# Kernel optimization log

Hardware: AMD Instinct MI355X
Metric: run time of the kernel (lower is better)

Reference implementation:

```python
import jax, jax.numpy as jnp
import numpy as np

B, S, D, H, N = 8, 1024, 1024, 16, 16  # batch, seq, hidden, heads, num_ns_tokens
HD = D // H


def setup_inputs() -> dict:
    key = jax.random.key(0)
    ks = jax.random.split(key, 8)
    s = 0.02
    return {
        "x": jax.random.normal(ks[0], (B, S, D), jnp.float32),
        "Wq_shared": jax.random.normal(ks[1], (D, D), jnp.float32) * s,
        "Wk_shared": jax.random.normal(ks[2], (D, D), jnp.float32) * s,
        "Wv_shared": jax.random.normal(ks[3], (D, D), jnp.float32) * s,
        "Wq_ded": jax.random.normal(ks[4], (N, D, D), jnp.float32) * s,
        "Wk_ded": jax.random.normal(ks[5], (N, D, D), jnp.float32) * s,
        "Wv_ded": jax.random.normal(ks[6], (N, D, D), jnp.float32) * s,
        "Wo": jax.random.normal(ks[7], (D, D), jnp.float32) * s,
    }


def reference(x, Wq_shared, Wk_shared, Wv_shared, Wq_ded, Wk_ded, Wv_ded, Wo):
    b, s, d = x.shape
    n = Wq_ded.shape[0]

    def proj(Ws, Wd):
        shared = x @ Ws                                   # [b,s,d]
        ded = jnp.einsum('bnd,ndo->bno', x[:, :n], Wd)    # first n tokens use dedicated weights
        return jnp.concatenate([ded, shared[:, n:]], axis=1)

    q = proj(Wq_shared, Wq_ded).reshape(b, s, H, HD)
    k = proj(Wk_shared, Wk_ded).reshape(b, s, H, HD)
    v = proj(Wv_shared, Wv_ded).reshape(b, s, H, HD)

    scores = jnp.einsum('bqhd,bkhd->bhqk', q, k) / jnp.sqrt(jnp.float32(HD))
    causal = jnp.tril(jnp.ones((s, s), dtype=bool))
    scores = jnp.where(causal, scores, jnp.float32(-1e9))
    attn = jax.nn.softmax(scores, axis=-1)
    out = jnp.einsum('bhqk,bkhd->bqhd', attn, v).reshape(b, s, d)
    output = out @ Wo
    return (output, k, v)
```

## Files before the change

### kernel.cpp

```cpp
#include <hip/hip_runtime.h>
#include <cstdint>


typedef unsigned short u16;
typedef __attribute__((ext_vector_type(8)))  __bf16 bf16x8;
typedef __attribute__((ext_vector_type(8)))  u16    u16x8;
typedef __attribute__((ext_vector_type(4)))  float  f32x4;

#define LOG2E 1.4426950408889634f
#define BSD   (8u * 1024u * 1024u)

__device__ __forceinline__ u16 f2bf(float f) {
    unsigned u = __builtin_bit_cast(unsigned, f);
    u += 0x7fffu + ((u >> 16) & 1u);
    return (u16)(u >> 16);
}

__device__ __forceinline__ void gl_lds16(const void* g, void* l) {
    __builtin_amdgcn_global_load_lds(
        (const __attribute__((address_space(1))) unsigned*)g,
        (__attribute__((address_space(3))) unsigned*)l, 16, 0, 0);
}

__global__ __launch_bounds__(256) void wt_convert(
        const float* __restrict__ Wq, const float* __restrict__ Wk,
        const float* __restrict__ Wv, const float* __restrict__ Wo,
        u16* __restrict__ WTcat, u16* __restrict__ WoT) {
    int z = blockIdx.z;
    const float* src = (z == 0) ? Wq : (z == 1) ? Wk : (z == 2) ? Wv : Wo;
    u16* dst = (z < 3) ? (WTcat + (size_t)z * 1024 * 1024) : WoT;
    int k0 = blockIdx.x * 32, n0 = blockIdx.y * 32;
    __shared__ float t[32][33];
    int x = threadIdx.x & 31, y = threadIdx.x >> 5;
#pragma unroll
    for (int i = 0; i < 4; ++i)
        t[y + 8 * i][x] = src[(size_t)(k0 + y + 8 * i) * 1024 + n0 + x];
    __syncthreads();
#pragma unroll
    for (int i = 0; i < 4; ++i)
        dst[(size_t)(n0 + y + 8 * i) * 1024 + k0 + x] = f2bf(t[x][y + 8 * i]);
}

__global__ __launch_bounds__(256) void x_convert(
        const float4* __restrict__ x, u16* __restrict__ xb) {
    int i = blockIdx.x * 256 + threadIdx.x;
    float4 v = x[i];
    ushort4 o;
    o.x = f2bf(v.x); o.y = f2bf(v.y); o.z = f2bf(v.z); o.w = f2bf(v.w);
    ((ushort4*)xb)[i] = o;
}

template <int MODE>
__global__ __launch_bounds__(256) void gemm128(
        const u16* __restrict__ A, const u16* __restrict__ Bt,
        float* __restrict__ fout, u16* __restrict__ q_attn,
        u16* __restrict__ k_attn, u16* __restrict__ vT) {
    const int K = 1024;
    __shared__ u16 As[128 * 32];
    __shared__ u16 Bs[128 * 32];
    int tid = threadIdx.x;
    int wave = tid >> 6, lane = tid & 63;
    int m0 = blockIdx.y * 128, n0 = blockIdx.x * 128;
    int wm = wave & 1, wn = wave >> 1;
    int lr = lane & 15, kg = lane >> 4;

    f32x4 acc[4][4] = {};

    int ci0 = wave * 128 + lane;
    int ci1 = ci0 + 64;

    for (int k0 = 0; k0 < K; k0 += 32) {
        __syncthreads();
        {
            int ci = ci0, row = ci >> 2, cg = (ci & 3) ^ ((row >> 1) & 3);
            gl_lds16(A  + (size_t)(m0 + row) * K + k0 + cg * 8, As + ci * 8);
            gl_lds16(Bt + (size_t)(n0 + row) * K + k0 + cg * 8, Bs + ci * 8);
            ci = ci1; row = ci >> 2; cg = (ci & 3) ^ ((row >> 1) & 3);
            gl_lds16(A  + (size_t)(m0 + row) * K + k0 + cg * 8, As + ci * 8);
            gl_lds16(Bt + (size_t)(n0 + row) * K + k0 + cg * 8, Bs + ci * 8);
        }
        __syncthreads();
        bf16x8 af[4], bf[4];
#pragma unroll
        for (int i = 0; i < 4; ++i) {
            int row = wm * 64 + i * 16 + lr;
            af[i] = __builtin_bit_cast(bf16x8,
                *(const u16x8*)&As[row * 32 + ((kg ^ ((row >> 1) & 3)) * 8)]);
        }
#pragma unroll
        for (int j = 0; j < 4; ++j) {
            int row = wn * 64 + j * 16 + lr;
            bf[j] = __builtin_bit_cast(bf16x8,
                *(const u16x8*)&Bs[row * 32 + ((kg ^ ((row >> 1) & 3)) * 8)]);
        }
#pragma unroll
        for (int i = 0; i < 4; ++i)
#pragma unroll
            for (int j = 0; j < 4; ++j)
                acc[i][j] = __builtin_amdgcn_mfma_f32_16x16x32_bf16(
                    af[i], bf[j], acc[i][j], 0, 0, 0);
    }

    if (MODE == 1) {
#pragma unroll
        for (int i = 0; i < 4; ++i) {
            int mbase = m0 + wm * 64 + i * 16 + kg * 4;
#pragma unroll
            for (int j = 0; j < 4; ++j) {
                int col = n0 + wn * 64 + j * 16 + lr;
#pragma unroll
                for (int r = 0; r < 4; ++r)
                    fout[(size_t)(mbase + r) * 1024 + col] = acc[i][j][r];
            }
        }
    } else {
        int matId = n0 >> 10;
        int ncol0 = (n0 & 1023) + wn * 64;
#pragma unroll
        for (int i = 0; i < 4; ++i) {
            int mbase = m0 + wm * 64 + i * 16 + kg * 4;
#pragma unroll
            for (int j = 0; j < 4; ++j) {
                int col = ncol0 + j * 16 + lr;
                int h = col >> 6, hd = col & 63;
#pragma unroll
                for (int r = 0; r < 4; ++r) {
                    int mm = mbase + r;
                    int b = mm >> 10, s = mm & 1023;
                    float v = acc[i][j][r];
                    size_t aidx = ((size_t)((b * 16 + h) * 1024 + s)) * 64 + hd;
                    if (matId == 0) {
                        q_attn[aidx] = f2bf(v * 0.125f);
                    } else if (matId == 1) {
                        fout[(size_t)BSD + (size_t)mm * 1024 + col] = v;
                        k_attn[aidx] = f2bf(v);
                    } else {
                        fout[(size_t)2 * BSD + (size_t)mm * 1024 + col] = v;
                        vT[((size_t)((b * 16 + h) * 64 + hd)) * 1024 + s] = f2bf(v);
                    }
                }
            }
        }
    }
}

__global__ __launch_bounds__(256) void ded_partial(
        const float* __restrict__ x, const float* __restrict__ Wq,
        const float* __restrict__ Wk, const float* __restrict__ Wv,
        float* __restrict__ part) {
    int dc = blockIdx.x, n = blockIdx.y, mat = blockIdx.z;
    const float* W = ((mat == 0) ? Wq : (mat == 1) ? Wk : Wv) +
                     (size_t)n * 1024 * 1024;
    __shared__ float xs[8 * 128];
    int t = threadIdx.x;
    for (int i = t; i < 1024; i += 256) {
        int b = i >> 7, d = i & 127;
        xs[i] = x[((size_t)b * 1024 + n) * 1024 + dc * 128 + d];
    }
    __syncthreads();
    int o0 = t * 4;
    float4 acc[8];
#pragma unroll
    for (int b = 0; b < 8; ++b) acc[b] = make_float4(0.f, 0.f, 0.f, 0.f);
    for (int d = 0; d < 128; ++d) {
        float4 w = *(const float4*)&W[(size_t)(dc * 128 + d) * 1024 + o0];
#pragma unroll
        for (int b = 0; b < 8; ++b) {
            float xv = xs[b * 128 + d];
            acc[b].x += xv * w.x; acc[b].y += xv * w.y;
            acc[b].z += xv * w.z; acc[b].w += xv * w.w;
        }
    }
#pragma unroll
    for (int b = 0; b < 8; ++b)
        *(float4*)&part[(size_t)(((mat * 8 + dc) * 8 + b) * 16 + n) * 1024 + o0] = acc[b];
}

__global__ __launch_bounds__(256) void ded_fixup(
        const float* __restrict__ part, float* __restrict__ d_out,
        u16* __restrict__ q_attn, u16* __restrict__ k_attn,
        u16* __restrict__ vT) {
    int blk = blockIdx.x;
    int mat = blk >> 7, b = (blk >> 4) & 7, n = blk & 15;
    int o0 = threadIdx.x * 4;
    float v[4] = {0.f, 0.f, 0.f, 0.f};
    for (int dc = 0; dc < 8; ++dc) {
        float4 p = *(const float4*)&part[(size_t)(((mat * 8 + dc) * 8 + b) * 16 + n) * 1024 + o0];
        v[0] += p.x; v[1] += p.y; v[2] += p.z; v[3] += p.w;
    }
#pragma unroll
    for (int j = 0; j < 4; ++j) {
        int col = o0 + j, h = col >> 6, hd = col & 63;
        size_t aidx = ((size_t)((b * 16 + h) * 1024 + n)) * 64 + hd;
        if (mat == 0) {
            q_attn[aidx] = f2bf(v[j] * 0.125f);
        } else if (mat == 1) {
            d_out[(size_t)BSD + ((size_t)b * 1024 + n) * 1024 + col] = v[j];
            k_attn[aidx] = f2bf(v[j]);
        } else {
            d_out[(size_t)2 * BSD + ((size_t)b * 1024 + n) * 1024 + col] = v[j];
            vT[((size_t)((b * 16 + h) * 64 + hd)) * 1024 + n] = f2bf(v[j]);
        }
    }
}

__global__ __launch_bounds__(256) void attn(
        const u16* __restrict__ q_attn, const u16* __restrict__ k_attn,
        const u16* __restrict__ vT, u16* __restrict__ O) {
    int qt = blockIdx.x, h = blockIdx.y, b = blockIdx.z;
    const u16* Qg = q_attn + (((size_t)(b * 16 + h) * 1024) + qt * 128) * 64;
    const u16* Kg = k_attn + ((size_t)(b * 16 + h) * 1024) * 64;
    const u16* Vg = vT + (size_t)(b * 16 + h) * 64 * 1024;

    __shared__ u16 Qs[128 * 64];
    __shared__ u16 Ks[64 * 64];
    __shared__ u16 Vs[64 * 64];
    __shared__ u16 Ps[128 * 64];
    __shared__ float red[4 * 32];

    int tid = threadIdx.x, wave = tid >> 6, lane = tid & 63;
    int lr = lane & 15, kg = lane >> 4;

#pragma unroll
    for (int j = 0; j < 4; ++j) {
        int ci = j * 256 + tid;
        int row = ci >> 3, cg = (ci & 7) ^ (row & 7);
        gl_lds16(Qg + (size_t)row * 64 + cg * 8, Qs + ci * 8);
    }

    float m_run[2] = {-1e30f, -1e30f};
    float l_run[2] = {0.f, 0.f};
    f32x4 oacc[2][4] = {};

    int nkt = 2 * qt + 2;
    for (int kt = 0; kt < nkt; ++kt) {
        __syncthreads();
#pragma unroll
        for (int j = 0; j < 2; ++j) {
            int ci = j * 256 + tid;
            int row = ci >> 3, cg = (ci & 7) ^ (row & 7);
            gl_lds16(Kg + ((size_t)(kt * 64 + row)) * 64 + cg * 8, Ks + ci * 8);
            gl_lds16(Vg + (size_t)row * 1024 + kt * 64 + cg * 8, Vs + ci * 8);
        }
        __syncthreads();

        f32x4 sacc[4][2] = {};
#pragma unroll
        for (int ks = 0; ks < 2; ++ks) {
            bf16x8 af[4], bq[2];
#pragma unroll
            for (int mi = 0; mi < 4; ++mi) {
                int row = mi * 16 + lr;
                af[mi] = __builtin_bit_cast(bf16x8,
                    *(const u16x8*)&Ks[row * 64 + (((ks * 4 + kg) ^ (row & 7)) * 8)]);
            }
#pragma unroll
            for (int nj = 0; nj < 2; ++nj) {
                int qr = wave * 32 + nj * 16 + lr;
                bq[nj] = __builtin_bit_cast(bf16x8,
                    *(const u16x8*)&Qs[qr * 64 + (((ks * 4 + kg) ^ (qr & 7)) * 8)]);
            }
#pragma unroll
            for (int mi = 0; mi < 4; ++mi)
#pragma unroll
                for (int nj = 0; nj < 2; ++nj)
                    sacc[mi][nj] = __builtin_amdgcn_mfma_f32_16x16x32_bf16(
                        af[mi], bq[nj], sacc[mi][nj], 0, 0, 0);
        }

        if (kt >= 2 * qt) {
#pragma unroll
            for (int mi = 0; mi < 4; ++mi)
#pragma unroll
                for (int nj = 0; nj < 2; ++nj)
#pragma unroll
                    for (int r = 0; r < 4; ++r) {
                        int kk_g = kt * 64 + mi * 16 + kg * 4 + r;
                        int q_g  = qt * 128 + wave * 32 + nj * 16 + lr;
                        if (kk_g > q_g) sacc[mi][nj][r] = -1e30f;
                    }
        }

        float alpha[2];
#pragma unroll
        for (int nj = 0; nj < 2; ++nj) {
            float mx = -1e30f;
#pragma unroll
            for (int mi = 0; mi < 4; ++mi)
#pragma unroll
                for (int r = 0; r < 4; ++r) mx = fmaxf(mx, sacc[mi][nj][r]);
            mx = fmaxf(mx, __shfl_xor(mx, 16));
            mx = fmaxf(mx, __shfl_xor(mx, 32));
            float mn = fmaxf(m_run[nj], mx);
            alpha[nj] = __builtin_amdgcn_exp2f((m_run[nj] - mn) * LOG2E);
            m_run[nj] = mn;
            float ps = 0.f;
            int q = wave * 32 + nj * 16 + lr;
#pragma unroll
            for (int mi = 0; mi < 4; ++mi) {
                float p0 = __builtin_amdgcn_exp2f((sacc[mi][nj][0] - mn) * LOG2E);
                float p1 = __builtin_amdgcn_exp2f((sacc[mi][nj][1] - mn) * LOG2E);
                float p2 = __builtin_amdgcn_exp2f((sacc[mi][nj][2] - mn) * LOG2E);
                float p3 = __builtin_amdgcn_exp2f((sacc[mi][nj][3] - mn) * LOG2E);
                ps += p0 + p1 + p2 + p3;
                int kkc = mi * 2 + (kg >> 1);
                int off = q * 64 + ((kkc ^ (q & 7)) * 8) + (kg & 1) * 4;
                uint2 w2;
                w2.x = (unsigned)f2bf(p0) | ((unsigned)f2bf(p1) << 16);
                w2.y = (unsigned)f2bf(p2) | ((unsigned)f2bf(p3) << 16);
                *(uint2*)&Ps[off] = w2;
            }
            ps += __shfl_xor(ps, 16);
            ps += __shfl_xor(ps, 32);
            l_run[nj] = l_run[nj] * alpha[nj] + ps;
            if (kg == 0) red[wave * 32 + nj * 16 + lr] = alpha[nj];
        }

#pragma unroll
        for (int mi = 0; mi < 2; ++mi) {
            f32x4 av = *(f32x4*)&red[wave * 32 + mi * 16 + kg * 4];
#pragma unroll
            for (int nj = 0; nj < 4; ++nj)
#pragma unroll
                for (int r = 0; r < 4; ++r) oacc[mi][nj][r] *= av[r];
        }
#pragma unroll
        for (int ks = 0; ks < 2; ++ks) {
            bf16x8 ap[2], bv[4];
#pragma unroll
            for (int mi = 0; mi < 2; ++mi) {
                int q = wave * 32 + mi * 16 + lr;
                ap[mi] = __builtin_bit_cast(bf16x8,
                    *(const u16x8*)&Ps[q * 64 + (((ks * 4 + kg) ^ (q & 7)) * 8)]);
            }
#pragma unroll
            for (int nj = 0; nj < 4; ++nj) {
                int hd = nj * 16 + lr;
                bv[nj] = __builtin_bit_cast(bf16x8,
                    *(const u16x8*)&Vs[hd * 64 + (((ks * 4 + kg) ^ (hd & 7)) * 8)]);
            }
#pragma unroll
            for (int mi = 0; mi < 2; ++mi)
#pragma unroll
                for (int nj = 0; nj < 4; ++nj)
                    oacc[mi][nj] = __builtin_amdgcn_mfma_f32_16x16x32_bf16(
                        ap[mi], bv[nj], oacc[mi][nj], 0, 0, 0);
        }
    }

    if (kg == 0) {
        red[wave * 32 + lr] = l_run[0];
        red[wave * 32 + 16 + lr] = l_run[1];
    }
#pragma unroll
    for (int mi = 0; mi < 2; ++mi) {
        f32x4 lv = *(f32x4*)&red[wave * 32 + mi * 16 + kg * 4];
        f32x4 rv;
#pragma unroll
        for (int r = 0; r < 4; ++r) rv[r] = __builtin_amdgcn_rcpf(lv[r]);
#pragma unroll
        for (int nj = 0; nj < 4; ++nj)
#pragma unroll
            for (int r = 0; r < 4; ++r) {
                int q_local = wave * 32 + mi * 16 + kg * 4 + r;
                size_t row = (size_t)b * 1024 + qt * 128 + q_local;
                O[row * 1024 + h * 64 + nj * 16 + lr] =
                    f2bf(oacc[mi][nj][r] * rv[r]);
            }
    }
}

extern "C" void kernel_launch(void* const* d_in, const int* in_sizes, int n_in,
                              void* d_out, int out_size, void* d_ws, size_t ws_size,
                              hipStream_t stream) {
    const float* x   = (const float*)d_in[0];
    const float* Wq  = (const float*)d_in[1];
    const float* Wk  = (const float*)d_in[2];
    const float* Wv  = (const float*)d_in[3];
    const float* Wqd = (const float*)d_in[4];
    const float* Wkd = (const float*)d_in[5];
    const float* Wvd = (const float*)d_in[6];
    const float* Wo  = (const float*)d_in[7];
    float* out = (float*)d_out;

    char* ws = (char*)d_ws;
    u16*   WTcat  = (u16*)(ws);
    u16*   WoT    = (u16*)(ws + 6291456);
    u16*   xb     = (u16*)(ws + 8388608);
    u16*   q_attn = (u16*)(ws + 25165824);
    u16*   k_attn = (u16*)(ws + 41943040);
    u16*   vT     = (u16*)(ws + 58720256);
    u16*   Ow     = (u16*)(ws + 75497472);
    float* part   = (float*)(ws + 92274688);

    wt_convert<<<dim3(32, 32, 4), 256, 0, stream>>>(Wq, Wk, Wv, Wo, WTcat, WoT);
    x_convert<<<dim3(8192), 256, 0, stream>>>((const float4*)x, xb);
    gemm128<0><<<dim3(24, 64), 256, 0, stream>>>(xb, WTcat, out, q_attn, k_attn, vT);
    ded_partial<<<dim3(8, 16, 3), 256, 0, stream>>>(x, Wqd, Wkd, Wvd, part);
    ded_fixup<<<dim3(384), 256, 0, stream>>>(part, out, q_attn, k_attn, vT);
    attn<<<dim3(8, 16, 8), 256, 0, stream>>>(q_attn, k_attn, vT, Ow);
    gemm128<1><<<dim3(8, 64), 256, 0, stream>>>(Ow, WoT, out, nullptr, nullptr, nullptr);
}
```

Before: 542.4 us.

## Move V transpose to separate kernel, fold log2e into Q scale, skip masked waves

```diff
diff --git a/kernel.cpp b/kernel.cpp
--- a/kernel.cpp
+++ b/kernel.cpp
@@ -7,8 +7,8 @@
 typedef __attribute__((ext_vector_type(8)))  u16    u16x8;
 typedef __attribute__((ext_vector_type(4)))  float  f32x4;
 
-#define LOG2E 1.4426950408889634f
 #define BSD   (8u * 1024u * 1024u)
+#define QSCALE 0.18033688011112042f
 
 __device__ __forceinline__ u16 f2bf(float f) {
     unsigned u = __builtin_bit_cast(unsigned, f);
@@ -54,7 +54,7 @@
 __global__ __launch_bounds__(256) void gemm128(
         const u16* __restrict__ A, const u16* __restrict__ Bt,
         float* __restrict__ fout, u16* __restrict__ q_attn,
-        u16* __restrict__ k_attn, u16* __restrict__ vT) {
+        u16* __restrict__ k_attn) {
     const int K = 1024;
     __shared__ u16 As[128 * 32];
     __shared__ u16 Bs[128 * 32];
@@ -130,13 +130,12 @@
                     float v = acc[i][j][r];
                     size_t aidx = ((size_t)((b * 16 + h) * 1024 + s)) * 64 + hd;
                     if (matId == 0) {
-                        q_attn[aidx] = f2bf(v * 0.125f);
+                        q_attn[aidx] = f2bf(v * QSCALE);
                     } else if (matId == 1) {
                         fout[(size_t)BSD + (size_t)mm * 1024 + col] = v;
                         k_attn[aidx] = f2bf(v);
                     } else {
                         fout[(size_t)2 * BSD + (size_t)mm * 1024 + col] = v;
-                        vT[((size_t)((b * 16 + h) * 64 + hd)) * 1024 + s] = f2bf(v);
                     }
                 }
             }
@@ -178,8 +177,7 @@
 
 __global__ __launch_bounds__(256) void ded_fixup(
         const float* __restrict__ part, float* __restrict__ d_out,
-        u16* __restrict__ q_attn, u16* __restrict__ k_attn,
-        u16* __restrict__ vT) {
+        u16* __restrict__ q_attn, u16* __restrict__ k_attn) {
     int blk = blockIdx.x;
     int mat = blk >> 7, b = (blk >> 4) & 7, n = blk & 15;
     int o0 = threadIdx.x * 4;
@@ -193,21 +191,51 @@
         int col = o0 + j, h = col >> 6, hd = col & 63;
         size_t aidx = ((size_t)((b * 16 + h) * 1024 + n)) * 64 + hd;
         if (mat == 0) {
-            q_attn[aidx] = f2bf(v[j] * 0.125f);
+            q_attn[aidx] = f2bf(v[j] * QSCALE);
         } else if (mat == 1) {
             d_out[(size_t)BSD + ((size_t)b * 1024 + n) * 1024 + col] = v[j];
             k_attn[aidx] = f2bf(v[j]);
         } else {
             d_out[(size_t)2 * BSD + ((size_t)b * 1024 + n) * 1024 + col] = v[j];
-            vT[((size_t)((b * 16 + h) * 64 + hd)) * 1024 + n] = f2bf(v[j]);
-        }
+        }
+    }
+}
+
+__global__ __launch_bounds__(256) void v_transpose(
+        const float* __restrict__ vf, u16* __restrict__ vT) {
+    int st = blockIdx.x, h = blockIdx.y, b = blockIdx.z;
+    __shared__ float t[64][65];
+    int tid = threadIdx.x;
+    int cg = tid & 15, sl = tid >> 4;
+#pragma unroll
+    for (int p = 0; p < 4; ++p) {
+        int s = p * 16 + sl;
+        float4 v = *(const float4*)&vf[
+            ((size_t)(b * 1024 + st * 64 + s)) * 1024 + h * 64 + cg * 4];
+        t[cg * 4 + 0][s] = v.x;
+        t[cg * 4 + 1][s] = v.y;
+        t[cg * 4 + 2][s] = v.z;
+        t[cg * 4 + 3][s] = v.w;
+    }
+    __syncthreads();
+    int hd = tid >> 2, sc = (tid & 3) * 16;
+    u16* dst = vT + ((size_t)((b * 16 + h) * 64 + hd)) * 1024 + st * 64 + sc;
+#pragma unroll
+    for (int c = 0; c < 4; ++c) {
+        ushort4 o;
+        o.x = f2bf(t[hd][sc + c * 4 + 0]);
+        o.y = f2bf(t[hd][sc + c * 4 + 1]);
+        o.z = f2bf(t[hd][sc + c * 4 + 2]);
+        o.w = f2bf(t[hd][sc + c * 4 + 3]);
+        *(ushort4*)(dst + c * 4) = o;
     }
 }
 
 __global__ __launch_bounds__(256) void attn(
         const u16* __restrict__ q_attn, const u16* __restrict__ k_attn,
         const u16* __restrict__ vT, u16* __restrict__ O) {
-    int qt = blockIdx.x, h = blockIdx.y, b = blockIdx.z;
+    int qt = 7 - blockIdx.x;
+    int h = blockIdx.y, b = blockIdx.z;
     const u16* Qg = q_attn + (((size_t)(b * 16 + h) * 1024) + qt * 128) * 64;
     const u16* Kg = k_attn + ((size_t)(b * 16 + h) * 1024) * 64;
     const u16* Vg = vT + (size_t)(b * 16 + h) * 64 * 1024;
@@ -244,107 +272,110 @@
         }
         __syncthreads();
 
-        f32x4 sacc[4][2] = {};
-#pragma unroll
-        for (int ks = 0; ks < 2; ++ks) {
-            bf16x8 af[4], bq[2];
-#pragma unroll
-            for (int mi = 0; mi < 4; ++mi) {
-                int row = mi * 16 + lr;
-                af[mi] = __builtin_bit_cast(bf16x8,
-                    *(const u16x8*)&Ks[row * 64 + (((ks * 4 + kg) ^ (row & 7)) * 8)]);
-            }
+        bool wactive = (qt * 128 + wave * 32 + 31) >= kt * 64;
+        if (wactive) {
+            f32x4 sacc[4][2] = {};
+#pragma unroll
+            for (int ks = 0; ks < 2; ++ks) {
+                bf16x8 af[4], bq[2];
+#pragma unroll
+                for (int mi = 0; mi < 4; ++mi) {
+                    int row = mi * 16 + lr;
+                    af[mi] = __builtin_bit_cast(bf16x8,
+                        *(const u16x8*)&Ks[row * 64 + (((ks * 4 + kg) ^ (row & 7)) * 8)]);
+                }
+#pragma unroll
+                for (int nj = 0; nj < 2; ++nj) {
+                    int qr = wave * 32 + nj * 16 + lr;
+                    bq[nj] = __builtin_bit_cast(bf16x8,
+                        *(const u16x8*)&Qs[qr * 64 + (((ks * 4 + kg) ^ (qr & 7)) * 8)]);
+                }
+#pragma unroll
+                for (int mi = 0; mi < 4; ++mi)
+#pragma unroll
+                    for (int nj = 0; nj < 2; ++nj)
+                        sacc[mi][nj] = __builtin_amdgcn_mfma_f32_16x16x32_bf16(
+                            af[mi], bq[nj], sacc[mi][nj], 0, 0, 0);
+            }
+
+            if (kt >= 2 * qt) {
+#pragma unroll
+                for (int mi = 0; mi < 4; ++mi)
+#pragma unroll
+                    for (int nj = 0; nj < 2; ++nj)
+#pragma unroll
+                        for (int r = 0; r < 4; ++r) {
+                            int kk_g = kt * 64 + mi * 16 + kg * 4 + r;
+                            int q_g  = qt * 128 + wave * 32 + nj * 16 + lr;
+                            if (kk_g > q_g) sacc[mi][nj][r] = -1e30f;
+                        }
+            }
+
+            float alpha[2];
 #pragma unroll
             for (int nj = 0; nj < 2; ++nj) {
-                int qr = wave * 32 + nj * 16 + lr;
-                bq[nj] = __builtin_bit_cast(bf16x8,
-                    *(const u16x8*)&Qs[qr * 64 + (((ks * 4 + kg) ^ (qr & 7)) * 8)]);
-            }
-#pragma unroll
-            for (int mi = 0; mi < 4; ++mi)
-#pragma unroll
-                for (int nj = 0; nj < 2; ++nj)
-                    sacc[mi][nj] = __builtin_amdgcn_mfma_f32_16x16x32_bf16(
-                        af[mi], bq[nj], sacc[mi][nj], 0, 0, 0);
-        }
-
-        if (kt >= 2 * qt) {
-#pragma unroll
-            for (int mi = 0; mi < 4; ++mi)
-#pragma unroll
-                for (int nj = 0; nj < 2; ++nj)
-#pragma unroll
-                    for (int r = 0; r < 4; ++r) {
-                        int kk_g = kt * 64 + mi * 16 + kg * 4 + r;
-                        int q_g  = qt * 128 + wave * 32 + nj * 16 + lr;
-                        if (kk_g > q_g) sacc[mi][nj][r] = -1e30f;
-                    }
-        }
-
-        float alpha[2];
-#pragma unroll
-        for (int nj = 0; nj < 2; ++nj) {
-            float mx = -1e30f;
-#pragma unroll
-            for (int mi = 0; mi < 4; ++mi)
-#pragma unroll
-                for (int r = 0; r < 4; ++r) mx = fmaxf(mx, sacc[mi][nj][r]);
-            mx = fmaxf(mx, __shfl_xor(mx, 16));
-            mx = fmaxf(mx, __shfl_xor(mx, 32));
-            float mn = fmaxf(m_run[nj], mx);
-            alpha[nj] = __builtin_amdgcn_exp2f((m_run[nj] - mn) * LOG2E);
-            m_run[nj] = mn;
-            float ps = 0.f;
-            int q = wave * 32 + nj * 16 + lr;
-#pragma unroll
-            for (int mi = 0; mi < 4; ++mi) {
-                float p0 = __builtin_amdgcn_exp2f((sacc[mi][nj][0] - mn) * LOG2E);
-                float p1 = __builtin_amdgcn_exp2f((sacc[mi][nj][1] - mn) * LOG2E);
-                float p2 = __builtin_amdgcn_exp2f((sacc[mi][nj][2] - mn) * LOG2E);
-                float p3 = __builtin_amdgcn_exp2f((sacc[mi][nj][3] - mn) * LOG2E);
-                ps += p0 + p1 + p2 + p3;
-                int kkc = mi * 2 + (kg >> 1);
-                int off = q * 64 + ((kkc ^ (q & 7)) * 8) + (kg & 1) * 4;
-                uint2 w2;
-                w2.x = (unsigned)f2bf(p0) | ((unsigned)f2bf(p1) << 16);
-                w2.y = (unsigned)f2bf(p2) | ((unsigned)f2bf(p3) << 16);
-                *(uint2*)&Ps[off] = w2;
-            }
-            ps += __shfl_xor(ps, 16);
-            ps += __shfl_xor(ps, 32);
-            l_run[nj] = l_run[nj] * alpha[nj] + ps;
-            if (kg == 0) red[wave * 32 + nj * 16 + lr] = alpha[nj];
-        }
-
-#pragma unroll
-        for (int mi = 0; mi < 2; ++mi) {
-            f32x4 av = *(f32x4*)&red[wave * 32 + mi * 16 + kg * 4];
-#pragma unroll
-            for (int nj = 0; nj < 4; ++nj)
-#pragma unroll
-                for (int r = 0; r < 4; ++r) oacc[mi][nj][r] *= av[r];
-        }
-#pragma unroll
-        for (int ks = 0; ks < 2; ++ks) {
-            bf16x8 ap[2], bv[4];
+                float mx = -1e30f;
+#pragma unroll
+                for (int mi = 0; mi < 4; ++mi)
+#pragma unroll
+                    for (int r = 0; r < 4; ++r) mx = fmaxf(mx, sacc[mi][nj][r]);
+                mx = fmaxf(mx, __shfl_xor(mx, 16));
+                mx = fmaxf(mx, __shfl_xor(mx, 32));
+                float mn = fmaxf(m_run[nj], mx);
+                alpha[nj] = __builtin_amdgcn_exp2f(m_run[nj] - mn);
+                m_run[nj] = mn;
+                float ps = 0.f;
+                int q = wave * 32 + nj * 16 + lr;
+#pragma unroll
+                for (int mi = 0; mi < 4; ++mi) {
+                    float p0 = __builtin_amdgcn_exp2f(sacc[mi][nj][0] - mn);
+                    float p1 = __builtin_amdgcn_exp2f(sacc[mi][nj][1] - mn);
+                    float p2 = __builtin_amdgcn_exp2f(sacc[mi][nj][2] - mn);
+                    float p3 = __builtin_amdgcn_exp2f(sacc[mi][nj][3] - mn);
+                    ps += p0 + p1 + p2 + p3;
+                    int kkc = mi * 2 + (kg >> 1);
+                    int off = q * 64 + ((kkc ^ (q & 7)) * 8) + (kg & 1) * 4;
+                    uint2 w2;
+                    w2.x = (unsigned)f2bf(p0) | ((unsigned)f2bf(p1) << 16);
+                    w2.y = (unsigned)f2bf(p2) | ((unsigned)f2bf(p3) << 16);
+                    *(uint2*)&Ps[off] = w2;
+                }
+                ps += __shfl_xor(ps, 16);
+                ps += __shfl_xor(ps, 32);
+                l_run[nj] = l_run[nj] * alpha[nj] + ps;
+                if (kg == 0) red[wave * 32 + nj * 16 + lr] = alpha[nj];
+            }
+
 #pragma unroll
             for (int mi = 0; mi < 2; ++mi) {
-                int q = wave * 32 + mi * 16 + lr;
-                ap[mi] = __builtin_bit_cast(bf16x8,
-                    *(const u16x8*)&Ps[q * 64 + (((ks * 4 + kg) ^ (q & 7)) * 8)]);
-            }
-#pragma unroll
-            for (int nj = 0; nj < 4; ++nj) {
-                int hd = nj * 16 + lr;
-                bv[nj] = __builtin_bit_cast(bf16x8,
-                    *(const u16x8*)&Vs[hd * 64 + (((ks * 4 + kg) ^ (hd & 7)) * 8)]);
-            }
-#pragma unroll
-            for (int mi = 0; mi < 2; ++mi)
+                f32x4 av = *(f32x4*)&red[wave * 32 + mi * 16 + kg * 4];
 #pragma unroll
                 for (int nj = 0; nj < 4; ++nj)
-                    oacc[mi][nj] = __builtin_amdgcn_mfma_f32_16x16x32_bf16(
-                        ap[mi], bv[nj], oacc[mi][nj], 0, 0, 0);
+#pragma unroll
+                    for (int r = 0; r < 4; ++r) oacc[mi][nj][r] *= av[r];
+            }
+#pragma unroll
+            for (int ks = 0; ks < 2; ++ks) {
+                bf16x8 ap[2], bv[4];
+#pragma unroll
+                for (int mi = 0; mi < 2; ++mi) {
+                    int q = wave * 32 + mi * 16 + lr;
+                    ap[mi] = __builtin_bit_cast(bf16x8,
+                        *(const u16x8*)&Ps[q * 64 + (((ks * 4 + kg) ^ (q & 7)) * 8)]);
+                }
+#pragma unroll
+                for (int nj = 0; nj < 4; ++nj) {
+                    int hd = nj * 16 + lr;
+                    bv[nj] = __builtin_bit_cast(bf16x8,
+                        *(const u16x8*)&Vs[hd * 64 + (((ks * 4 + kg) ^ (hd & 7)) * 8)]);
+                }
+#pragma unroll
+                for (int mi = 0; mi < 2; ++mi)
+#pragma unroll
+                    for (int nj = 0; nj < 4; ++nj)
+                        oacc[mi][nj] = __builtin_amdgcn_mfma_f32_16x16x32_bf16(
+                            ap[mi], bv[nj], oacc[mi][nj], 0, 0, 0);
+            }
         }
     }
 
@@ -395,9 +426,10 @@
 
     wt_convert<<<dim3(32, 32, 4), 256, 0, stream>>>(Wq, Wk, Wv, Wo, WTcat, WoT);
     x_convert<<<dim3(8192), 256, 0, stream>>>((const float4*)x, xb);
-    gemm128<0><<<dim3(24, 64), 256, 0, stream>>>(xb, WTcat, out, q_attn, k_attn, vT);
+    gemm128<0><<<dim3(24, 64), 256, 0, stream>>>(xb, WTcat, out, q_attn, k_attn);
     ded_partial<<<dim3(8, 16, 3), 256, 0, stream>>>(x, Wqd, Wkd, Wvd, part);
-    ded_fixup<<<dim3(384), 256, 0, stream>>>(part, out, q_attn, k_attn, vT);
+    ded_fixup<<<dim3(384), 256, 0, stream>>>(part, out, q_attn, k_attn);
+    v_transpose<<<dim3(16, 16, 8), 256, 0, stream>>>(out + (size_t)2 * BSD, vT);
     attn<<<dim3(8, 16, 8), 256, 0, stream>>>(q_attn, k_attn, vT, Ow);
-    gemm128<1><<<dim3(8, 64), 256, 0, stream>>>(Ow, WoT, out, nullptr, nullptr, nullptr);
-}
+    gemm128<1><<<dim3(8, 64), 256, 0, stream>>>(Ow, WoT, out, nullptr, nullptr);
+}
```

After: 519.0 us. -4.3%, faster.
